# Kernel optimization log

Measured on AMD Instinct MI355X. Metric: run time of the kernel, lower is better.

The kernel has to match this reference:

```python
import jax, jax.numpy as jnp
import numpy as np

B, S = 256, 512
MEM, DK, DV, DS = 32, 128, 128, 256
NQ = 10000
ABILITY_SCALE = 3.0


def _kaiming(key, shape, fan_in):
    return jax.random.normal(key, shape, dtype=jnp.float32) * jnp.sqrt(2.0 / fan_in)


def setup_inputs() -> dict:
    key = jax.random.key(0)
    ks = jax.random.split(key, 20)
    q_data = jax.random.randint(ks[0], (B, S), 0, NQ + 1)
    qa_data = jax.random.randint(ks[1], (B, S), 0, 2 * NQ + 1)
    # embedding tables (padding_idx=0 row zeroed)
    q_table = _kaiming(ks[2], (NQ + 1, DK), DK).at[0].set(0.0)
    qa_table = _kaiming(ks[3], (2 * NQ + 1, DV), DV).at[0].set(0.0)
    # DKVMN memories
    key_memory = _kaiming(ks[4], (MEM, DK), DK)
    init_value_memory = _kaiming(ks[5], (MEM, DV), DV)
    # DKVMN write transforms (erase: sigmoid, add: tanh)
    W_erase = _kaiming(ks[6], (DV, DV), DV); b_erase = jnp.zeros((DV,), jnp.float32)
    W_add = _kaiming(ks[7], (DV, DV), DV); b_add = jnp.zeros((DV,), jnp.float32)
    # summary network: Linear(DV+DK -> DS) + tanh
    W_sum = _kaiming(ks[8], (DV + DK, DS), DV + DK); b_sum = jnp.zeros((DS,), jnp.float32)
    # student ability net: Linear(DS->DS)+tanh, Linear(DS->1)
    W_ab1 = _kaiming(ks[9], (DS, DS), DS); b_ab1 = jnp.zeros((DS,), jnp.float32)
    W_ab2 = _kaiming(ks[10], (DS, 1), DS); b_ab2 = jnp.zeros((1,), jnp.float32)
    # item difficulty net: Linear(DK->DK)+tanh, Linear(DK->1)
    W_df1 = _kaiming(ks[11], (DK, DK), DK); b_df1 = jnp.zeros((DK,), jnp.float32)
    W_df2 = _kaiming(ks[12], (DK, 1), DK); b_df2 = jnp.zeros((1,), jnp.float32)
    return dict(q_data=q_data, qa_data=qa_data, q_table=q_table, qa_table=qa_table,
                key_memory=key_memory, init_value_memory=init_value_memory,
                W_erase=W_erase, b_erase=b_erase, W_add=W_add, b_add=b_add,
                W_sum=W_sum, b_sum=b_sum, W_ab1=W_ab1, b_ab1=b_ab1,
                W_ab2=W_ab2, b_ab2=b_ab2, W_df1=W_df1, b_df1=b_df1,
                W_df2=W_df2, b_df2=b_df2)


def _forward(q_data, qa_data, q_table, qa_table, key_memory, init_value_memory,
             W_erase, b_erase, W_add, b_add, W_sum, b_sum,
             W_ab1, b_ab1, W_ab2, b_ab2, W_df1, b_df1, W_df2, b_df2):
    qe = q_table[q_data]            # [B,S,DK]
    qae = qa_table[qa_data]         # [B,S,DV]
    # attention weights for every timestep (depend only on q embeddings)
    w_all = jax.nn.softmax(jnp.einsum('bsd,md->bsm', qe, key_memory), axis=-1)  # [B,S,M]
    erase = jax.nn.sigmoid(qae @ W_erase + b_erase)   # [B,S,DV]
    add = jnp.tanh(qae @ W_add + b_add)               # [B,S,DV]
    Mv0 = jnp.broadcast_to(init_value_memory, (q_data.shape[0], MEM, DV))

    def step(Mv, xs):
        w, e, a = xs  # [B,M], [B,DV], [B,DV]
        read = jnp.einsum('bm,bmd->bd', w, Mv)  # read BEFORE write
        Mv = Mv * (1.0 - w[:, :, None] * e[:, None, :]) + w[:, :, None] * a[:, None, :]
        return Mv, read

    xs = (jnp.swapaxes(w_all, 0, 1), jnp.swapaxes(erase, 0, 1), jnp.swapaxes(add, 0, 1))
    _, reads = jax.lax.scan(step, Mv0, xs)          # reads: [S,B,DV]
    reads = jnp.swapaxes(reads, 0, 1)               # [B,S,DV]

    summary = jnp.tanh(jnp.concatenate([reads, qe], axis=-1) @ W_sum + b_sum)  # [B,S,DS]
    ability = jnp.tanh(summary @ W_ab1 + b_ab1) @ W_ab2 + b_ab2                # [B,S,1]
    difficulty = jnp.tanh(qe @ W_df1 + b_df1) @ W_df2 + b_df2                  # [B,S,1]
    z = ABILITY_SCALE * ability - difficulty
    pred = jax.nn.sigmoid(z)
    return (pred[..., 0], ability[..., 0], difficulty[..., 0], z[..., 0])


def reference(q_data, qa_data, q_table, qa_table, key_memory, init_value_memory,
              W_erase, b_erase, W_add, b_add, W_sum, b_sum,
              W_ab1, b_ab1, W_ab2, b_ab2, W_df1, b_df1, W_df2, b_df2):
    return _forward(q_data, qa_data, q_table, qa_table, key_memory, init_value_memory,
                    W_erase, b_erase, W_add, b_add, W_sum, b_sum,
                    W_ab1, b_ab1, W_ab2, b_ab2, W_df1, b_df1, W_df2, b_df2)
```

## Files before the change

### kernel.cpp

```cpp
#include <hip/hip_runtime.h>
#include <hip/hip_bf16.h>

typedef unsigned short u16;
typedef unsigned int   u32;

#define B_N   256
#define S_N   512
#define BSN   (B_N * S_N)
#define MEMN  32
#define DKN   128
#define DVN   128
#define DSN   256

typedef __attribute__((ext_vector_type(8))) short bf16x8;
typedef __attribute__((ext_vector_type(4))) float f32x4;

__device__ __forceinline__ float bf2f(u16 u) {
  union { u32 i; float f; } v; v.i = ((u32)u) << 16; return v.f;
}
__device__ __forceinline__ u16 f2bf(float f) {
  union { float f; u32 i; } v; v.f = f;
  u32 x = v.i;
  x += 0x7fffu + ((x >> 16) & 1u);
  return (u16)(x >> 16);
}
__device__ __forceinline__ u32 pack2(float a, float b) {
  return (u32)f2bf(a) | ((u32)f2bf(b) << 16);
}
__device__ __forceinline__ float sigmoid_fast(float x) { return 1.f / (1.f + __expf(-x)); }
__device__ __forceinline__ float tanh_fast(float x)    { return 1.f - 2.f / (__expf(2.f * x) + 1.f); }

#define GLOAD_LDS16(g, l)                                         \
  __builtin_amdgcn_global_load_lds(                               \
      (const __attribute__((address_space(1))) void*)(g),         \
      (__attribute__((address_space(3))) void*)(l), 16, 0, 0)

__global__ __launch_bounds__(256) void kPrep(
    const float* __restrict__ W_sum, const float* __restrict__ W_ab1,
    const float* __restrict__ W_er,  const float* __restrict__ W_ad,
    const float* __restrict__ key_mem, const float* __restrict__ W_df1,
    u16* __restrict__ WsumT, u16* __restrict__ Wab1T,
    u16* __restrict__ WerT,  u16* __restrict__ WaddT,
    u16* __restrict__ BqT)
{
  int e = blockIdx.x * 256 + threadIdx.x;
  if (e < 65536) {
    const int n = e >> 8, k = e & 255;
    WsumT[e] = f2bf(W_sum[k * 256 + n]);
  } else if (e < 131072) {
    e -= 65536;
    const int n = e >> 8, k = e & 255;
    Wab1T[e] = f2bf(W_ab1[k * 256 + n]);
  } else if (e < 147456) {
    e -= 131072;
    const int n = e >> 7, k = e & 127;
    WerT[e] = f2bf(W_er[k * 128 + n]);
  } else if (e < 163840) {
    e -= 147456;
    const int n = e >> 7, k = e & 127;
    WaddT[e] = f2bf(W_ad[k * 128 + n]);
  } else if (e < 184320) {
    e -= 163840;
    const int n = e >> 7, k = e & 127;
    BqT[e] = f2bf(n < 32 ? key_mem[n * 128 + k] : W_df1[k * 128 + (n - 32)]);
  }
}

__global__ __launch_bounds__(256) void kErAdd(
    const int* __restrict__ qa_data, const float* __restrict__ qa_table,
    const u16* __restrict__ WerT, const u16* __restrict__ WaddT,
    const float* __restrict__ b_er, const float* __restrict__ b_ad,
    u16* __restrict__ eras, u16* __restrict__ addb)
{
  __shared__ __align__(16) u16 As[4 * 128 * 32];
  __shared__ __align__(16) u16 Bs[2 * 128 * 32];
  const int tid = threadIdx.x;
  const int p0  = blockIdx.x * 128;
  const int sel = blockIdx.y;
  const u16*   Wt = sel ? WaddT : WerT;
  const float* bb = sel ? b_ad  : b_er;
  u16*       outp = sel ? addb  : eras;

  {
    const int r = tid >> 1, h = tid & 1;
    const long base = (long)qa_data[p0 + r] * DVN + h * 64;
    #pragma unroll
    for (int g = 0; g < 8; ++g) {
      const int k0 = h * 64 + g * 8;
      const float4 fa = *(const float4*)(qa_table + base + g * 8);
      const float4 fb = *(const float4*)(qa_table + base + g * 8 + 4);
      uint4 pk;
      pk.x = pack2(fa.x, fa.y); pk.y = pack2(fa.z, fa.w);
      pk.z = pack2(fb.x, fb.y); pk.w = pack2(fb.z, fb.w);
      *(uint4*)(As + (k0 >> 5) * 4096 + r * 32 + (k0 & 31)) = pk;
    }
  }
  {
    #pragma unroll
    for (int u = 0; u < 2; ++u) {
      const int f = tid + 256 * u;
      const int n = f >> 2, j = f & 3;
      *(uint4*)(Bs + n * 32 + j * 8) = *(const uint4*)(Wt + n * 128 + j * 8);
    }
  }
  __syncthreads();

  const int lane = tid & 63, wave = tid >> 6;
  const int wr = (wave >> 1) * 64, wc = (wave & 1) * 64;
  const int c15 = lane & 15, q = lane >> 4;

  f32x4 acc[4][4];
  #pragma unroll
  for (int b = 0; b < 4; ++b) {
    const float bv = bb[wc + 16 * b + c15];
    #pragma unroll
    for (int a = 0; a < 4; ++a) acc[a][b] = (f32x4){bv, bv, bv, bv};
  }

  for (int c = 0; c < 4; ++c) {
    const int cur = c & 1;
    uint4 st[2];
    const bool more = (c + 1 < 4);
    if (more) {
      #pragma unroll
      for (int u = 0; u < 2; ++u) {
        const int f = tid + 256 * u;
        const int n = f >> 2, j = f & 3;
        st[u] = *(const uint4*)(Wt + n * 128 + (c + 1) * 32 + j * 8);
      }
    }
    bf16x8 af[4], bf[4];
    #pragma unroll
    for (int a = 0; a < 4; ++a)
      af[a] = *(const bf16x8*)(As + c * 4096 + (wr + 16 * a + c15) * 32 + q * 8);
    #pragma unroll
    for (int b = 0; b < 4; ++b)
      bf[b] = *(const bf16x8*)(Bs + cur * 4096 + (wc + 16 * b + c15) * 32 + q * 8);
    #pragma unroll
    for (int a = 0; a < 4; ++a)
      #pragma unroll
      for (int b = 0; b < 4; ++b)
        acc[a][b] = __builtin_amdgcn_mfma_f32_16x16x32_bf16(af[a], bf[b], acc[a][b], 0, 0, 0);
    if (more) {
      #pragma unroll
      for (int u = 0; u < 2; ++u) {
        const int f = tid + 256 * u;
        const int n = f >> 2, j = f & 3;
        *(uint4*)(Bs + (cur ^ 1) * 4096 + n * 32 + j * 8) = st[u];
      }
    }
    __syncthreads();
  }

  const int colb = wc + c15;
  #pragma unroll
  for (int a = 0; a < 4; ++a) {
    #pragma unroll
    for (int r = 0; r < 4; ++r) {
      const int row = p0 + wr + 16 * a + 4 * q + r;
      u16* yp = outp + (long)row * DVN + colb;
      #pragma unroll
      for (int b = 0; b < 4; ++b) {
        const float v = sel ? tanh_fast(acc[a][b][r]) : sigmoid_fast(acc[a][b][r]);
        yp[16 * b] = f2bf(v);
      }
    }
  }
}

__global__ __launch_bounds__(256) void kSum(
    const u16* __restrict__ X, const u16* __restrict__ WsumT,
    const float* __restrict__ bias, u16* __restrict__ Y)
{
  __shared__ __align__(16) u16 As[8 * 128 * 32];
  __shared__ __align__(16) u16 Bs[2 * 128 * 32];
  const int tid = threadIdx.x;
  const int p0  = blockIdx.x * 128;
  const int j0  = blockIdx.y * 128;

  {
    #pragma unroll
    for (int u = 0; u < 16; ++u) {
      const int f = tid + 256 * u;
      const int r = f >> 5, j = f & 31;
      const uint4 raw = *(const uint4*)(X + (long)(p0 + r) * DSN + j * 8);
      *(uint4*)(As + (j >> 2) * 4096 + r * 32 + (j & 3) * 8) = raw;
    }
  }
  {
    #pragma unroll
    for (int u = 0; u < 2; ++u) {
      const int f = tid + 256 * u;
      const int n = f >> 2, j = f & 3;
      *(uint4*)(Bs + n * 32 + j * 8) = *(const uint4*)(WsumT + (j0 + n) * 256 + j * 8);
    }
  }
  __syncthreads();

  const int lane = tid & 63, wave = tid >> 6;
  const int wr = (wave >> 1) * 64, wc = (wave & 1) * 64;
  const int c15 = lane & 15, q = lane >> 4;

  f32x4 acc[4][4];
  #pragma unroll
  for (int b = 0; b < 4; ++b) {
    const float bv = bias[j0 + wc + 16 * b + c15];
    #pragma unroll
    for (int a = 0; a < 4; ++a) acc[a][b] = (f32x4){bv, bv, bv, bv};
  }

  for (int c = 0; c < 8; ++c) {
    const int cur = c & 1;
    uint4 st[2];
    const bool more = (c + 1 < 8);
    if (more) {
      #pragma unroll
      for (int u = 0; u < 2; ++u) {
        const int f = tid + 256 * u;
        const int n = f >> 2, j = f & 3;
        st[u] = *(const uint4*)(WsumT + (j0 + n) * 256 + (c + 1) * 32 + j * 8);
      }
    }
    bf16x8 af[4], bf[4];
    #pragma unroll
    for (int a = 0; a < 4; ++a)
      af[a] = *(const bf16x8*)(As + c * 4096 + (wr + 16 * a + c15) * 32 + q * 8);
    #pragma unroll
    for (int b = 0; b < 4; ++b)
      bf[b] = *(const bf16x8*)(Bs + cur * 4096 + (wc + 16 * b + c15) * 32 + q * 8);
    #pragma unroll
    for (int a = 0; a < 4; ++a)
      #pragma unroll
      for (int b = 0; b < 4; ++b)
        acc[a][b] = __builtin_amdgcn_mfma_f32_16x16x32_bf16(af[a], bf[b], acc[a][b], 0, 0, 0);
    if (more) {
      #pragma unroll
      for (int u = 0; u < 2; ++u) {
        const int f = tid + 256 * u;
        const int n = f >> 2, j = f & 3;
        *(uint4*)(Bs + (cur ^ 1) * 4096 + n * 32 + j * 8) = st[u];
      }
    }
    __syncthreads();
  }

  const int colb = j0 + wc + c15;
  #pragma unroll
  for (int a = 0; a < 4; ++a) {
    #pragma unroll
    for (int r = 0; r < 4; ++r) {
      const int row = p0 + wr + 16 * a + 4 * q + r;
      u16* yp = Y + (long)row * DSN + colb;
      #pragma unroll
      for (int b = 0; b < 4; ++b)
        yp[16 * b] = f2bf(tanh_fast(acc[a][b][r]));
    }
  }
}

__global__ __launch_bounds__(256) void kAb(
    const u16* __restrict__ X, const u16* __restrict__ Wab1T,
    const float* __restrict__ bias, const float* __restrict__ Wab2,
    float* __restrict__ part)
{
  __shared__ __align__(16) u16 As[8 * 128 * 32];
  __shared__ __align__(16) u16 Bs[2 * 128 * 32];
  const int tid = threadIdx.x;
  const int p0  = blockIdx.x * 128;
  const int j0  = blockIdx.y * 128;

  {
    #pragma unroll
    for (int u = 0; u < 16; ++u) {
      const int f = tid + 256 * u;
      const int r = f >> 5, j = f & 31;
      const uint4 raw = *(const uint4*)(X + (long)(p0 + r) * DSN + j * 8);
      *(uint4*)(As + (j >> 2) * 4096 + r * 32 + (j & 3) * 8) = raw;
    }
  }
  {
    #pragma unroll
    for (int u = 0; u < 2; ++u) {
      const int f = tid + 256 * u;
      const int n = f >> 2, j = f & 3;
      *(uint4*)(Bs + n * 32 + j * 8) = *(const uint4*)(Wab1T + (j0 + n) * 256 + j * 8);
    }
  }
  __syncthreads();

  const int lane = tid & 63, wave = tid >> 6;
  const int wr = (wave >> 1) * 64, wc = (wave & 1) * 64;
  const int c15 = lane & 15, q = lane >> 4;

  f32x4 acc[4][4];
  float w2v[4];
  #pragma unroll
  for (int b = 0; b < 4; ++b) {
    const int col = j0 + wc + 16 * b + c15;
    const float bv = bias[col];
    w2v[b] = Wab2[col];
    #pragma unroll
    for (int a = 0; a < 4; ++a) acc[a][b] = (f32x4){bv, bv, bv, bv};
  }

  for (int c = 0; c < 8; ++c) {
    const int cur = c & 1;
    uint4 st[2];
    const bool more = (c + 1 < 8);
    if (more) {
      #pragma unroll
      for (int u = 0; u < 2; ++u) {
        const int f = tid + 256 * u;
        const int n = f >> 2, j = f & 3;
        st[u] = *(const uint4*)(Wab1T + (j0 + n) * 256 + (c + 1) * 32 + j * 8);
      }
    }
    bf16x8 af[4], bf[4];
    #pragma unroll
    for (int a = 0; a < 4; ++a)
      af[a] = *(const bf16x8*)(As + c * 4096 + (wr + 16 * a + c15) * 32 + q * 8);
    #pragma unroll
    for (int b = 0; b < 4; ++b)
      bf[b] = *(const bf16x8*)(Bs + cur * 4096 + (wc + 16 * b + c15) * 32 + q * 8);
    #pragma unroll
    for (int a = 0; a < 4; ++a)
      #pragma unroll
      for (int b = 0; b < 4; ++b)
        acc[a][b] = __builtin_amdgcn_mfma_f32_16x16x32_bf16(af[a], bf[b], acc[a][b], 0, 0, 0);
    if (more) {
      #pragma unroll
      for (int u = 0; u < 2; ++u) {
        const int f = tid + 256 * u;
        const int n = f >> 2, j = f & 3;
        *(uint4*)(Bs + (cur ^ 1) * 4096 + n * 32 + j * 8) = st[u];
      }
    }
    __syncthreads();
  }

  float sv[4][4];
  #pragma unroll
  for (int a = 0; a < 4; ++a) {
    #pragma unroll
    for (int r = 0; r < 4; ++r) {
      float s = 0.f;
      #pragma unroll
      for (int b = 0; b < 4; ++b)
        s = fmaf(tanh_fast(acc[a][b][r]), w2v[b], s);
      s += __shfl_xor(s, 1, 64);
      s += __shfl_xor(s, 2, 64);
      s += __shfl_xor(s, 4, 64);
      s += __shfl_xor(s, 8, 64);
      sv[a][r] = s;
    }
  }
  float* red = (float*)Bs;
  if ((wave & 1) && c15 == 0) {
    #pragma unroll
    for (int a = 0; a < 4; ++a)
      #pragma unroll
      for (int r = 0; r < 4; ++r)
        red[wr + 16 * a + 4 * q + r] = sv[a][r];
  }
  __syncthreads();
  if (!(wave & 1) && c15 == 0) {
    #pragma unroll
    for (int a = 0; a < 4; ++a)
      #pragma unroll
      for (int r = 0; r < 4; ++r) {
        const int rr = wr + 16 * a + 4 * q + r;
        part[(long)blockIdx.y * BSN + p0 + rr] = sv[a][r] + red[rr];
      }
  }
}

__global__ __launch_bounds__(256) void kQe(
    const int* __restrict__ q_data, const float* __restrict__ q_table,
    const u16* __restrict__ BqT,
    const float* __restrict__ bdf1, const float* __restrict__ Wdf2,
    const float* __restrict__ bdf2,
    float* __restrict__ w_all, float* __restrict__ diff,
    u16* __restrict__ sin_buf)
{
  __shared__ __align__(16) u16 As[4 * 128 * 32];
  __shared__ __align__(16) u16 Bs[4 * 160 * 32];
  const int tid = threadIdx.x;
  const int p0  = blockIdx.x * 128;

  {
    const int r = tid >> 1, h = tid & 1;
    const long base = (long)q_data[p0 + r] * DKN + h * 64;
    #pragma unroll
    for (int g = 0; g < 8; ++g) {
      const int k0 = h * 64 + g * 8;
      const float4 fa = *(const float4*)(q_table + base + g * 8);
      const float4 fb = *(const float4*)(q_table + base + g * 8 + 4);
      uint4 pk;
      pk.x = pack2(fa.x, fa.y); pk.y = pack2(fa.z, fa.w);
      pk.z = pack2(fb.x, fb.y); pk.w = pack2(fb.z, fb.w);
      *(uint4*)(As + (k0 >> 5) * 4096 + r * 32 + (k0 & 31)) = pk;
      *(uint4*)(sin_buf + (long)(p0 + r) * DSN + DKN + k0) = pk;
    }
  }
  {
    #pragma unroll
    for (int u = 0; u < 10; ++u) {
      const int f = tid + 256 * u;
      const int n = f >> 4, jj = f & 15;
      *(uint4*)(Bs + (jj >> 2) * 5120 + n * 32 + (jj & 3) * 8) =
          *(const uint4*)(BqT + n * 128 + jj * 8);
    }
  }
  __syncthreads();

  const int lane = tid & 63, wave = tid >> 6;
  const int wr = (wave >> 1) * 64, wc = (wave & 1) * 80;
  const int c15 = lane & 15, q = lane >> 4;

  f32x4 acc[4][5];
  float w2v[5];
  #pragma unroll
  for (int b = 0; b < 5; ++b) {
    const int col = wc + 16 * b + c15;
    const float bv = (col < 32) ? 0.f : bdf1[col - 32];
    w2v[b] = (col < 32) ? 0.f : Wdf2[col - 32];
    #pragma unroll
    for (int a = 0; a < 4; ++a) acc[a][b] = (f32x4){bv, bv, bv, bv};
  }

  #pragma unroll
  for (int c = 0; c < 4; ++c) {
    bf16x8 af[4], bf[5];
    #pragma unroll
    for (int a = 0; a < 4; ++a)
      af[a] = *(const bf16x8*)(As + c * 4096 + (wr + 16 * a + c15) * 32 + q * 8);
    #pragma unroll
    for (int b = 0; b < 5; ++b)
      bf[b] = *(const bf16x8*)(Bs + c * 5120 + (wc + 16 * b + c15) * 32 + q * 8);
    #pragma unroll
    for (int a = 0; a < 4; ++a)
      #pragma unroll
      for (int b = 0; b < 5; ++b)
        acc[a][b] = __builtin_amdgcn_mfma_f32_16x16x32_bf16(af[a], bf[b], acc[a][b], 0, 0, 0);
  }

  if (wc == 0) {
    #pragma unroll
    for (int a = 0; a < 4; ++a) {
      #pragma unroll
      for (int r = 0; r < 4; ++r) {
        float s0 = acc[a][0][r], s1 = acc[a][1][r];
        float mx = fmaxf(s0, s1);
        mx = fmaxf(mx, __shfl_xor(mx, 1, 64));
        mx = fmaxf(mx, __shfl_xor(mx, 2, 64));
        mx = fmaxf(mx, __shfl_xor(mx, 4, 64));
        mx = fmaxf(mx, __shfl_xor(mx, 8, 64));
        const float e0 = __expf(s0 - mx), e1 = __expf(s1 - mx);
        float sm = e0 + e1;
        sm += __shfl_xor(sm, 1, 64);
        sm += __shfl_xor(sm, 2, 64);
        sm += __shfl_xor(sm, 4, 64);
        sm += __shfl_xor(sm, 8, 64);
        const float inv = 1.f / sm;
        const int row = p0 + wr + 16 * a + 4 * q + r;
        w_all[(long)row * MEMN + c15]      = e0 * inv;
        w_all[(long)row * MEMN + 16 + c15] = e1 * inv;
      }
    }
  }

  float sv[4][4];
  #pragma unroll
  for (int a = 0; a < 4; ++a) {
    #pragma unroll
    for (int r = 0; r < 4; ++r) {
      float s = 0.f;
      #pragma unroll
      for (int b = 0; b < 5; ++b)
        s = fmaf(tanh_fast(acc[a][b][r]), w2v[b], s);
      s += __shfl_xor(s, 1, 64);
      s += __shfl_xor(s, 2, 64);
      s += __shfl_xor(s, 4, 64);
      s += __shfl_xor(s, 8, 64);
      sv[a][r] = s;
    }
  }
  __syncthreads();
  float* red = (float*)As;
  if ((wave & 1) && c15 == 0) {
    #pragma unroll
    for (int a = 0; a < 4; ++a)
      #pragma unroll
      for (int r = 0; r < 4; ++r)
        red[wr + 16 * a + 4 * q + r] = sv[a][r];
  }
  __syncthreads();
  if (!(wave & 1) && c15 == 0) {
    const float bd = bdf2[0];
    #pragma unroll
    for (int a = 0; a < 4; ++a)
      #pragma unroll
      for (int r = 0; r < 4; ++r) {
        const int rr = wr + 16 * a + 4 * q + r;
        diff[p0 + rr] = sv[a][r] + red[rr] + bd;
      }
  }
}

#define CHUNK_BYTES 12288
#define PB_OFF      25088

#define KSTAGE(K, BUF)                                                        \
  {                                                                           \
    const char* wsrc = (const char*)(w_all + (pbase + (long)(K) * 32) * MEMN);\
    const char* esrc = (const char*)(eras + (pbase + (long)(K) * 32) * DVN)   \
                       + ch * 128;                                            \
    const char* asrc = (const char*)(addb + (pbase + (long)(K) * 32) * DVN)   \
                       + ch * 128;                                            \
    char* dst = lds + (BUF) * CHUNK_BYTES;                                    \
    _Pragma("unroll")                                                         \
    for (int r = 0; r < 3; ++r) {                                             \
      const int o = (tid + r * 256) * 16;                                     \
      const char* src;                                                        \
      if (o < 4096) {                                                         \
        src = wsrc + o;                                                       \
      } else if (o < 8192) {                                                  \
        const int f = o - 4096;                                               \
        src = esrc + (f >> 7) * 256 + (f & 127);                              \
      } else {                                                                \
        const int f = o - 8192;                                               \
        src = asrc + (f >> 7) * 256 + (f & 127);                              \
      }                                                                       \
      GLOAD_LDS16(src, dst + o);                                              \
    }                                                                         \
  }

__global__ __launch_bounds__(256) void kScan(
    const float* __restrict__ w_all, const u16* __restrict__ eras,
    const u16* __restrict__ addb, const float* __restrict__ init_mem,
    u16* __restrict__ sin_buf)
{
  __shared__ __align__(16) char lds[PB_OFF + 32768];
  const int tid = threadIdx.x;
  const int ch  = blockIdx.x & 1;
  const int lc  = tid >> 2;
  const int gc  = ch * 64 + lc;
  const int h   = tid & 3;
  const long pbase = (long)(blockIdx.x >> 1) * S_N;

  float* pb = (float*)(lds + PB_OFF);

  float Mv[8];
  #pragma unroll
  for (int m = 0; m < 8; ++m) Mv[m] = init_mem[(h * 8 + m) * DVN + gc];

  const int lc2  = tid & 63;
  const int sblk = tid >> 6;
  u16* sp2 = sin_buf + pbase * DSN + ch * 64 + lc2;

  KSTAGE(0, 0)
  for (int k = 0; k < 16; ++k) {
    __syncthreads();
    if (k + 1 < 16) KSTAGE(k + 1, (k + 1) & 1)

    const char*  wb  = lds + (k & 1) * CHUNK_BYTES;
    const f32x4* wl4 = (const f32x4*)wb;
    const u16*   el  = (const u16*)(wb + 4096);
    const u16*   al  = (const u16*)(wb + 8192);

    f32x4 Wr[3][2];
    u16 er[3], ar[3];
    #pragma unroll
    for (int i = 0; i < 2; ++i) Wr[0][i] = wl4[h * 2 + i];
    er[0] = el[lc]; ar[0] = al[lc];
    #pragma unroll
    for (int i = 0; i < 2; ++i) Wr[1][i] = wl4[8 + h * 2 + i];
    er[1] = el[64 + lc]; ar[1] = al[64 + lc];

    #pragma unroll
    for (int s = 0; s < 32; ++s) {
      const int cur = s % 3, nx2 = (s + 2) % 3;
      Wr[nx2][0] = wl4[(s + 2) * 8 + h * 2];
      Wr[nx2][1] = wl4[(s + 2) * 8 + h * 2 + 1];
      er[nx2] = el[(s + 2) * 64 + lc];
      ar[nx2] = al[(s + 2) * 64 + lc];
      {
        float ac0 = 0.f, ac1 = 0.f, ac2 = 0.f, ac3 = 0.f;
        #pragma unroll
        for (int i = 0; i < 2; ++i) {
          ac0 = fmaf(Wr[cur][i][0], Mv[4 * i + 0], ac0);
          ac1 = fmaf(Wr[cur][i][1], Mv[4 * i + 1], ac1);
          ac2 = fmaf(Wr[cur][i][2], Mv[4 * i + 2], ac2);
          ac3 = fmaf(Wr[cur][i][3], Mv[4 * i + 3], ac3);
        }
        pb[s * 256 + lc * 4 + h] = (ac0 + ac1) + (ac2 + ac3);
        const float ec = bf2f(er[cur]);
        const float an = -bf2f(ar[cur]);
        #pragma unroll
        for (int i = 0; i < 2; ++i) {
          #pragma unroll
          for (int j = 0; j < 4; ++j) {
            const float t = fmaf(ec, Mv[4 * i + j], an);
            Mv[4 * i + j] = fmaf(-Wr[cur][i][j], t, Mv[4 * i + j]);
          }
        }
      }
    }

    __syncthreads();
    const int lb = k * 32;
    #pragma unroll
    for (int r = 0; r < 8; ++r) {
      const int s = sblk * 8 + r;
      const f32x4 pv = *(const f32x4*)(pb + s * 256 + lc2 * 4);
      sp2[(long)(lb + s) * DSN] = f2bf((pv[0] + pv[1]) + (pv[2] + pv[3]));
    }
  }
}

__global__ __launch_bounds__(256) void kOut(
    const float* __restrict__ part, const float* __restrict__ diff,
    const float* __restrict__ bab2, float* __restrict__ out)
{
  const int p = blockIdx.x * 256 + threadIdx.x;
  const float ab = part[p] + part[BSN + p] + bab2[0];
  const float d  = diff[p];
  const float z  = 3.0f * ab - d;
  out[p]           = sigmoid_fast(z);
  out[BSN + p]     = ab;
  out[2 * BSN + p] = d;
  out[3 * BSN + p] = z;
}

extern "C" void kernel_launch(void* const* d_in, const int* in_sizes, int n_in,
                              void* d_out, int out_size, void* d_ws, size_t ws_size,
                              hipStream_t stream)
{
  const int*   q_data   = (const int*)d_in[0];
  const int*   qa_data  = (const int*)d_in[1];
  const float* q_table  = (const float*)d_in[2];
  const float* qa_table = (const float*)d_in[3];
  const float* key_mem  = (const float*)d_in[4];
  const float* init_mem = (const float*)d_in[5];
  const float* W_erase  = (const float*)d_in[6];
  const float* b_erase  = (const float*)d_in[7];
  const float* W_add    = (const float*)d_in[8];
  const float* b_add    = (const float*)d_in[9];
  const float* W_sum    = (const float*)d_in[10];
  const float* b_sum    = (const float*)d_in[11];
  const float* W_ab1    = (const float*)d_in[12];
  const float* b_ab1    = (const float*)d_in[13];
  const float* W_ab2    = (const float*)d_in[14];
  const float* b_ab2    = (const float*)d_in[15];
  const float* W_df1    = (const float*)d_in[16];
  const float* b_df1    = (const float*)d_in[17];
  const float* W_df2    = (const float*)d_in[18];
  const float* b_df2    = (const float*)d_in[19];

  char* ws = (char*)d_ws;
  float* w_all = (float*)(ws + 0);
  u16*   eras  = (u16*)(ws + 16777216);
  u16*   addb  = (u16*)(ws + 50331648);
  u16*   sinb  = (u16*)(ws + 83886080);
  float* diffb = (float*)(ws + 150994944);
  float* part  = (float*)(ws + 151519232);
  u16*   WerT  = (u16*)(ws + 152567808);
  u16*   WaddT = (u16*)(ws + 152600576);
  u16*   WsumT = (u16*)(ws + 152633344);
  u16*   Wab1T = (u16*)(ws + 152764416);
  u16*   BqT   = (u16*)(ws + 152895488);
  u16*   summ  = eras;

  kPrep<<<dim3(720), 256, 0, stream>>>(W_sum, W_ab1, W_erase, W_add, key_mem, W_df1,
                                       WsumT, Wab1T, WerT, WaddT, BqT);
  kErAdd<<<dim3(BSN / 128, 2), 256, 0, stream>>>(qa_data, qa_table, WerT, WaddT,
                                                 b_erase, b_add, eras, addb);
  kQe<<<dim3(BSN / 128), 256, 0, stream>>>(q_data, q_table, BqT, b_df1, W_df2, b_df2,
                                           w_all, diffb, sinb);
  kScan<<<dim3(B_N * 2), 256, 0, stream>>>(w_all, eras, addb, init_mem, sinb);
  kSum<<<dim3(BSN / 128, 2), 256, 0, stream>>>(sinb, WsumT, b_sum, summ);
  kAb<<<dim3(BSN / 128, 2), 256, 0, stream>>>(summ, Wab1T, b_ab1, W_ab2, part);
  kOut<<<dim3(BSN / 256), 256, 0, stream>>>(part, diffb, b_ab2, (float*)d_out);
}
```

Measured before the change: 353.1 us.

## Fuse summary, ability and output kernels; compute erase and add in one block

The summary GEMM, ability GEMM and output epilogue are merged into one kernel that keeps the 128x256 tanh summary tile in shared memory and reuses it as the A operand of the second GEMM. This removes the global round trip of the summary activations and the partial-sum buffer, and drops two launches. Separately, kErAdd now loops over erase and add inside each block so the gathered qa embeddings are loaded once instead of twice. The trade-offs are higher register pressure (32 accumulators per wave), single-buffered weight staging with an extra barrier per k-step, and half as many blocks.

```diff
diff --git a/kernel.cpp b/kernel.cpp
--- a/kernel.cpp
+++ b/kernel.cpp
@@ -76,10 +76,6 @@
   __shared__ __align__(16) u16 Bs[2 * 128 * 32];
   const int tid = threadIdx.x;
   const int p0  = blockIdx.x * 128;
-  const int sel = blockIdx.y;
-  const u16*   Wt = sel ? WaddT : WerT;
-  const float* bb = sel ? b_ad  : b_er;
-  u16*       outp = sel ? addb  : eras;
 
   {
     const int r = tid >> 1, h = tid & 1;
@@ -95,282 +91,83 @@
       *(uint4*)(As + (k0 >> 5) * 4096 + r * 32 + (k0 & 31)) = pk;
     }
   }
-  {
-    #pragma unroll
-    for (int u = 0; u < 2; ++u) {
-      const int f = tid + 256 * u;
-      const int n = f >> 2, j = f & 3;
-      *(uint4*)(Bs + n * 32 + j * 8) = *(const uint4*)(Wt + n * 128 + j * 8);
-    }
-  }
-  __syncthreads();
 
   const int lane = tid & 63, wave = tid >> 6;
   const int wr = (wave >> 1) * 64, wc = (wave & 1) * 64;
   const int c15 = lane & 15, q = lane >> 4;
 
-  f32x4 acc[4][4];
-  #pragma unroll
-  for (int b = 0; b < 4; ++b) {
-    const float bv = bb[wc + 16 * b + c15];
-    #pragma unroll
-    for (int a = 0; a < 4; ++a) acc[a][b] = (f32x4){bv, bv, bv, bv};
-  }
-
-  for (int c = 0; c < 4; ++c) {
-    const int cur = c & 1;
-    uint4 st[2];
-    const bool more = (c + 1 < 4);
-    if (more) {
+  for (int sel = 0; sel < 2; ++sel) {
+    const u16*   Wt = sel ? WaddT : WerT;
+    const float* bb = sel ? b_ad  : b_er;
+    u16*       outp = sel ? addb  : eras;
+
+    {
       #pragma unroll
       for (int u = 0; u < 2; ++u) {
         const int f = tid + 256 * u;
         const int n = f >> 2, j = f & 3;
-        st[u] = *(const uint4*)(Wt + n * 128 + (c + 1) * 32 + j * 8);
-      }
-    }
-    bf16x8 af[4], bf[4];
-    #pragma unroll
-    for (int a = 0; a < 4; ++a)
-      af[a] = *(const bf16x8*)(As + c * 4096 + (wr + 16 * a + c15) * 32 + q * 8);
-    #pragma unroll
-    for (int b = 0; b < 4; ++b)
-      bf[b] = *(const bf16x8*)(Bs + cur * 4096 + (wc + 16 * b + c15) * 32 + q * 8);
-    #pragma unroll
-    for (int a = 0; a < 4; ++a)
+        *(uint4*)(Bs + n * 32 + j * 8) = *(const uint4*)(Wt + n * 128 + j * 8);
+      }
+    }
+    __syncthreads();
+
+    f32x4 acc[4][4];
+    #pragma unroll
+    for (int b = 0; b < 4; ++b) {
+      const float bv = bb[wc + 16 * b + c15];
+      #pragma unroll
+      for (int a = 0; a < 4; ++a) acc[a][b] = (f32x4){bv, bv, bv, bv};
+    }
+
+    for (int c = 0; c < 4; ++c) {
+      const int cur = c & 1;
+      uint4 st[2];
+      const bool more = (c + 1 < 4);
+      if (more) {
+        #pragma unroll
+        for (int u = 0; u < 2; ++u) {
+          const int f = tid + 256 * u;
+          const int n = f >> 2, j = f & 3;
+          st[u] = *(const uint4*)(Wt + n * 128 + (c + 1) * 32 + j * 8);
+        }
+      }
+      bf16x8 af[4], bf[4];
+      #pragma unroll
+      for (int a = 0; a < 4; ++a)
+        af[a] = *(const bf16x8*)(As + c * 4096 + (wr + 16 * a + c15) * 32 + q * 8);
       #pragma unroll
       for (int b = 0; b < 4; ++b)
-        acc[a][b] = __builtin_amdgcn_mfma_f32_16x16x32_bf16(af[a], bf[b], acc[a][b], 0, 0, 0);
-    if (more) {
-      #pragma unroll
-      for (int u = 0; u < 2; ++u) {
-        const int f = tid + 256 * u;
-        const int n = f >> 2, j = f & 3;
-        *(uint4*)(Bs + (cur ^ 1) * 4096 + n * 32 + j * 8) = st[u];
-      }
-    }
-    __syncthreads();
-  }
-
-  const int colb = wc + c15;
-  #pragma unroll
-  for (int a = 0; a < 4; ++a) {
-    #pragma unroll
-    for (int r = 0; r < 4; ++r) {
-      const int row = p0 + wr + 16 * a + 4 * q + r;
-      u16* yp = outp + (long)row * DVN + colb;
-      #pragma unroll
-      for (int b = 0; b < 4; ++b) {
-        const float v = sel ? tanh_fast(acc[a][b][r]) : sigmoid_fast(acc[a][b][r]);
-        yp[16 * b] = f2bf(v);
-      }
-    }
-  }
-}
-
-__global__ __launch_bounds__(256) void kSum(
-    const u16* __restrict__ X, const u16* __restrict__ WsumT,
-    const float* __restrict__ bias, u16* __restrict__ Y)
-{
-  __shared__ __align__(16) u16 As[8 * 128 * 32];
-  __shared__ __align__(16) u16 Bs[2 * 128 * 32];
-  const int tid = threadIdx.x;
-  const int p0  = blockIdx.x * 128;
-  const int j0  = blockIdx.y * 128;
-
-  {
-    #pragma unroll
-    for (int u = 0; u < 16; ++u) {
-      const int f = tid + 256 * u;
-      const int r = f >> 5, j = f & 31;
-      const uint4 raw = *(const uint4*)(X + (long)(p0 + r) * DSN + j * 8);
-      *(uint4*)(As + (j >> 2) * 4096 + r * 32 + (j & 3) * 8) = raw;
-    }
-  }
-  {
-    #pragma unroll
-    for (int u = 0; u < 2; ++u) {
-      const int f = tid + 256 * u;
-      const int n = f >> 2, j = f & 3;
-      *(uint4*)(Bs + n * 32 + j * 8) = *(const uint4*)(WsumT + (j0 + n) * 256 + j * 8);
-    }
-  }
-  __syncthreads();
-
-  const int lane = tid & 63, wave = tid >> 6;
-  const int wr = (wave >> 1) * 64, wc = (wave & 1) * 64;
-  const int c15 = lane & 15, q = lane >> 4;
-
-  f32x4 acc[4][4];
-  #pragma unroll
-  for (int b = 0; b < 4; ++b) {
-    const float bv = bias[j0 + wc + 16 * b + c15];
-    #pragma unroll
-    for (int a = 0; a < 4; ++a) acc[a][b] = (f32x4){bv, bv, bv, bv};
-  }
-
-  for (int c = 0; c < 8; ++c) {
-    const int cur = c & 1;
-    uint4 st[2];
-    const bool more = (c + 1 < 8);
-    if (more) {
-      #pragma unroll
-      for (int u = 0; u < 2; ++u) {
-        const int f = tid + 256 * u;
-        const int n = f >> 2, j = f & 3;
-        st[u] = *(const uint4*)(WsumT + (j0 + n) * 256 + (c + 1) * 32 + j * 8);
-      }
-    }
-    bf16x8 af[4], bf[4];
-    #pragma unroll
-    for (int a = 0; a < 4; ++a)
-      af[a] = *(const bf16x8*)(As + c * 4096 + (wr + 16 * a + c15) * 32 + q * 8);
-    #pragma unroll
-    for (int b = 0; b < 4; ++b)
-      bf[b] = *(const bf16x8*)(Bs + cur * 4096 + (wc + 16 * b + c15) * 32 + q * 8);
-    #pragma unroll
-    for (int a = 0; a < 4; ++a)
-      #pragma unroll
-      for (int b = 0; b < 4; ++b)
-        acc[a][b] = __builtin_amdgcn_mfma_f32_16x16x32_bf16(af[a], bf[b], acc[a][b], 0, 0, 0);
-    if (more) {
-      #pragma unroll
-      for (int u = 0; u < 2; ++u) {
-        const int f = tid + 256 * u;
-        const int n = f >> 2, j = f & 3;
-        *(uint4*)(Bs + (cur ^ 1) * 4096 + n * 32 + j * 8) = st[u];
-      }
-    }
-    __syncthreads();
-  }
-
-  const int colb = j0 + wc + c15;
-  #pragma unroll
-  for (int a = 0; a < 4; ++a) {
-    #pragma unroll
-    for (int r = 0; r < 4; ++r) {
-      const int row = p0 + wr + 16 * a + 4 * q + r;
-      u16* yp = Y + (long)row * DSN + colb;
-      #pragma unroll
-      for (int b = 0; b < 4; ++b)
-        yp[16 * b] = f2bf(tanh_fast(acc[a][b][r]));
-    }
-  }
-}
-
-__global__ __launch_bounds__(256) void kAb(
-    const u16* __restrict__ X, const u16* __restrict__ Wab1T,
-    const float* __restrict__ bias, const float* __restrict__ Wab2,
-    float* __restrict__ part)
-{
-  __shared__ __align__(16) u16 As[8 * 128 * 32];
-  __shared__ __align__(16) u16 Bs[2 * 128 * 32];
-  const int tid = threadIdx.x;
-  const int p0  = blockIdx.x * 128;
-  const int j0  = blockIdx.y * 128;
-
-  {
-    #pragma unroll
-    for (int u = 0; u < 16; ++u) {
-      const int f = tid + 256 * u;
-      const int r = f >> 5, j = f & 31;
-      const uint4 raw = *(const uint4*)(X + (long)(p0 + r) * DSN + j * 8);
-      *(uint4*)(As + (j >> 2) * 4096 + r * 32 + (j & 3) * 8) = raw;
-    }
-  }
-  {
-    #pragma unroll
-    for (int u = 0; u < 2; ++u) {
-      const int f = tid + 256 * u;
-      const int n = f >> 2, j = f & 3;
-      *(uint4*)(Bs + n * 32 + j * 8) = *(const uint4*)(Wab1T + (j0 + n) * 256 + j * 8);
-    }
-  }
-  __syncthreads();
-
-  const int lane = tid & 63, wave = tid >> 6;
-  const int wr = (wave >> 1) * 64, wc = (wave & 1) * 64;
-  const int c15 = lane & 15, q = lane >> 4;
-
-  f32x4 acc[4][4];
-  float w2v[4];
-  #pragma unroll
-  for (int b = 0; b < 4; ++b) {
-    const int col = j0 + wc + 16 * b + c15;
-    const float bv = bias[col];
-    w2v[b] = Wab2[col];
-    #pragma unroll
-    for (int a = 0; a < 4; ++a) acc[a][b] = (f32x4){bv, bv, bv, bv};
-  }
-
-  for (int c = 0; c < 8; ++c) {
-    const int cur = c & 1;
-    uint4 st[2];
-    const bool more = (c + 1 < 8);
-    if (more) {
-      #pragma unroll
-      for (int u = 0; u < 2; ++u) {
-        const int f = tid + 256 * u;
-        const int n = f >> 2, j = f & 3;
-        st[u] = *(const uint4*)(Wab1T + (j0 + n) * 256 + (c + 1) * 32 + j * 8);
-      }
-    }
-    bf16x8 af[4], bf[4];
-    #pragma unroll
-    for (int a = 0; a < 4; ++a)
-      af[a] = *(const bf16x8*)(As + c * 4096 + (wr + 16 * a + c15) * 32 + q * 8);
-    #pragma unroll
-    for (int b = 0; b < 4; ++b)
-      bf[b] = *(const bf16x8*)(Bs + cur * 4096 + (wc + 16 * b + c15) * 32 + q * 8);
-    #pragma unroll
-    for (int a = 0; a < 4; ++a)
-      #pragma unroll
-      for (int b = 0; b < 4; ++b)
-        acc[a][b] = __builtin_amdgcn_mfma_f32_16x16x32_bf16(af[a], bf[b], acc[a][b], 0, 0, 0);
-    if (more) {
-      #pragma unroll
-      for (int u = 0; u < 2; ++u) {
-        const int f = tid + 256 * u;
-        const int n = f >> 2, j = f & 3;
-        *(uint4*)(Bs + (cur ^ 1) * 4096 + n * 32 + j * 8) = st[u];
-      }
-    }
-    __syncthreads();
-  }
-
-  float sv[4][4];
-  #pragma unroll
-  for (int a = 0; a < 4; ++a) {
-    #pragma unroll
-    for (int r = 0; r < 4; ++r) {
-      float s = 0.f;
-      #pragma unroll
-      for (int b = 0; b < 4; ++b)
-        s = fmaf(tanh_fast(acc[a][b][r]), w2v[b], s);
-      s += __shfl_xor(s, 1, 64);
-      s += __shfl_xor(s, 2, 64);
-      s += __shfl_xor(s, 4, 64);
-      s += __shfl_xor(s, 8, 64);
-      sv[a][r] = s;
-    }
-  }
-  float* red = (float*)Bs;
-  if ((wave & 1) && c15 == 0) {
-    #pragma unroll
-    for (int a = 0; a < 4; ++a)
-      #pragma unroll
-      for (int r = 0; r < 4; ++r)
-        red[wr + 16 * a + 4 * q + r] = sv[a][r];
-  }
-  __syncthreads();
-  if (!(wave & 1) && c15 == 0) {
-    #pragma unroll
-    for (int a = 0; a < 4; ++a)
+        bf[b] = *(const bf16x8*)(Bs + cur * 4096 + (wc + 16 * b + c15) * 32 + q * 8);
+      #pragma unroll
+      for (int a = 0; a < 4; ++a)
+        #pragma unroll
+        for (int b = 0; b < 4; ++b)
+          acc[a][b] = __builtin_amdgcn_mfma_f32_16x16x32_bf16(af[a], bf[b], acc[a][b], 0, 0, 0);
+      if (more) {
+        #pragma unroll
+        for (int u = 0; u < 2; ++u) {
+          const int f = tid + 256 * u;
+          const int n = f >> 2, j = f & 3;
+          *(uint4*)(Bs + (cur ^ 1) * 4096 + n * 32 + j * 8) = st[u];
+        }
+      }
+      __syncthreads();
+    }
+
+    const int colb = wc + c15;
+    #pragma unroll
+    for (int a = 0; a < 4; ++a) {
       #pragma unroll
       for (int r = 0; r < 4; ++r) {
-        const int rr = wr + 16 * a + 4 * q + r;
-        part[(long)blockIdx.y * BSN + p0 + rr] = sv[a][r] + red[rr];
-      }
+        const int row = p0 + wr + 16 * a + 4 * q + r;
+        u16* yp = outp + (long)row * DVN + colb;
+        #pragma unroll
+        for (int b = 0; b < 4; ++b) {
+          const float v = sel ? tanh_fast(acc[a][b][r]) : sigmoid_fast(acc[a][b][r]);
+          yp[16 * b] = f2bf(v);
+        }
+      }
+    }
   }
 }
 
@@ -618,18 +415,192 @@
   }
 }
 
-__global__ __launch_bounds__(256) void kOut(
-    const float* __restrict__ part, const float* __restrict__ diff,
-    const float* __restrict__ bab2, float* __restrict__ out)
+__global__ __launch_bounds__(256) void kSumAb(
+    const u16* __restrict__ X, const u16* __restrict__ WsumT,
+    const float* __restrict__ bsum, const u16* __restrict__ Wab1T,
+    const float* __restrict__ bab1, const float* __restrict__ Wab2,
+    const float* __restrict__ bab2, const float* __restrict__ diffb,
+    float* __restrict__ out)
 {
-  const int p = blockIdx.x * 256 + threadIdx.x;
-  const float ab = part[p] + part[BSN + p] + bab2[0];
-  const float d  = diff[p];
-  const float z  = 3.0f * ab - d;
-  out[p]           = sigmoid_fast(z);
-  out[BSN + p]     = ab;
-  out[2 * BSN + p] = d;
-  out[3 * BSN + p] = z;
+  __shared__ __align__(16) u16 As[8 * 128 * 32];
+  __shared__ __align__(16) u16 Bs[256 * 32];
+  const int tid = threadIdx.x;
+  const int p0  = blockIdx.x * 128;
+
+  {
+    #pragma unroll
+    for (int u = 0; u < 16; ++u) {
+      const int f = tid + 256 * u;
+      const int r = f >> 5, j = f & 31;
+      const uint4 raw = *(const uint4*)(X + (long)(p0 + r) * DSN + j * 8);
+      *(uint4*)(As + (j >> 2) * 4096 + r * 32 + (j & 3) * 8) = raw;
+    }
+  }
+  {
+    #pragma unroll
+    for (int u = 0; u < 4; ++u) {
+      const int f = tid + 256 * u;
+      const int n = f >> 2, j = f & 3;
+      *(uint4*)(Bs + n * 32 + j * 8) = *(const uint4*)(WsumT + n * 256 + j * 8);
+    }
+  }
+  __syncthreads();
+
+  const int lane = tid & 63, wave = tid >> 6;
+  const int wr = (wave >> 1) * 64, wc = (wave & 1) * 128;
+  const int c15 = lane & 15, q = lane >> 4;
+
+  f32x4 acc[4][8];
+  #pragma unroll
+  for (int b = 0; b < 8; ++b) {
+    const float bv = bsum[wc + 16 * b + c15];
+    #pragma unroll
+    for (int a = 0; a < 4; ++a) acc[a][b] = (f32x4){bv, bv, bv, bv};
+  }
+
+  for (int c = 0; c < 8; ++c) {
+    uint4 st[4];
+    const bool more = (c + 1 < 8);
+    if (more) {
+      #pragma unroll
+      for (int u = 0; u < 4; ++u) {
+        const int f = tid + 256 * u;
+        const int n = f >> 2, j = f & 3;
+        st[u] = *(const uint4*)(WsumT + n * 256 + (c + 1) * 32 + j * 8);
+      }
+    }
+    bf16x8 af[4], bf[8];
+    #pragma unroll
+    for (int a = 0; a < 4; ++a)
+      af[a] = *(const bf16x8*)(As + c * 4096 + (wr + 16 * a + c15) * 32 + q * 8);
+    #pragma unroll
+    for (int b = 0; b < 8; ++b)
+      bf[b] = *(const bf16x8*)(Bs + (wc + 16 * b + c15) * 32 + q * 8);
+    #pragma unroll
+    for (int a = 0; a < 4; ++a)
+      #pragma unroll
+      for (int b = 0; b < 8; ++b)
+        acc[a][b] = __builtin_amdgcn_mfma_f32_16x16x32_bf16(af[a], bf[b], acc[a][b], 0, 0, 0);
+    __syncthreads();
+    if (more) {
+      #pragma unroll
+      for (int u = 0; u < 4; ++u) {
+        const int f = tid + 256 * u;
+        const int n = f >> 2, j = f & 3;
+        *(uint4*)(Bs + n * 32 + j * 8) = st[u];
+      }
+      __syncthreads();
+    }
+  }
+
+  #pragma unroll
+  for (int a = 0; a < 4; ++a)
+    #pragma unroll
+    for (int b = 0; b < 8; ++b) {
+      const int col = wc + 16 * b + c15;
+      u16* sp = As + (col >> 5) * 4096 + (col & 31);
+      #pragma unroll
+      for (int r = 0; r < 4; ++r) {
+        const int row = wr + 16 * a + 4 * q + r;
+        sp[row * 32] = f2bf(tanh_fast(acc[a][b][r]));
+      }
+    }
+  {
+    #pragma unroll
+    for (int u = 0; u < 4; ++u) {
+      const int f = tid + 256 * u;
+      const int n = f >> 2, j = f & 3;
+      *(uint4*)(Bs + n * 32 + j * 8) = *(const uint4*)(Wab1T + n * 256 + j * 8);
+    }
+  }
+  __syncthreads();
+
+  float w2v[8];
+  #pragma unroll
+  for (int b = 0; b < 8; ++b) {
+    const int col = wc + 16 * b + c15;
+    const float bv = bab1[col];
+    w2v[b] = Wab2[col];
+    #pragma unroll
+    for (int a = 0; a < 4; ++a) acc[a][b] = (f32x4){bv, bv, bv, bv};
+  }
+  for (int c = 0; c < 8; ++c) {
+    uint4 st[4];
+    const bool more = (c + 1 < 8);
+    if (more) {
+      #pragma unroll
+      for (int u = 0; u < 4; ++u) {
+        const int f = tid + 256 * u;
+        const int n = f >> 2, j = f & 3;
+        st[u] = *(const uint4*)(Wab1T + n * 256 + (c + 1) * 32 + j * 8);
+      }
+    }
+    bf16x8 af[4], bf[8];
+    #pragma unroll
+    for (int a = 0; a < 4; ++a)
+      af[a] = *(const bf16x8*)(As + c * 4096 + (wr + 16 * a + c15) * 32 + q * 8);
+    #pragma unroll
+    for (int b = 0; b < 8; ++b)
+      bf[b] = *(const bf16x8*)(Bs + (wc + 16 * b + c15) * 32 + q * 8);
+    #pragma unroll
+    for (int a = 0; a < 4; ++a)
+      #pragma unroll
+      for (int b = 0; b < 8; ++b)
+        acc[a][b] = __builtin_amdgcn_mfma_f32_16x16x32_bf16(af[a], bf[b], acc[a][b], 0, 0, 0);
+    __syncthreads();
+    if (more) {
+      #pragma unroll
+      for (int u = 0; u < 4; ++u) {
+        const int f = tid + 256 * u;
+        const int n = f >> 2, j = f & 3;
+        *(uint4*)(Bs + n * 32 + j * 8) = st[u];
+      }
+      __syncthreads();
+    }
+  }
+
+  float sv[4][4];
+  #pragma unroll
+  for (int a = 0; a < 4; ++a) {
+    #pragma unroll
+    for (int r = 0; r < 4; ++r) {
+      float s = 0.f;
+      #pragma unroll
+      for (int b = 0; b < 8; ++b)
+        s = fmaf(tanh_fast(acc[a][b][r]), w2v[b], s);
+      s += __shfl_xor(s, 1, 64);
+      s += __shfl_xor(s, 2, 64);
+      s += __shfl_xor(s, 4, 64);
+      s += __shfl_xor(s, 8, 64);
+      sv[a][r] = s;
+    }
+  }
+  float* red = (float*)Bs;
+  if ((wave & 1) && c15 == 0) {
+    #pragma unroll
+    for (int a = 0; a < 4; ++a)
+      #pragma unroll
+      for (int r = 0; r < 4; ++r)
+        red[wr + 16 * a + 4 * q + r] = sv[a][r];
+  }
+  __syncthreads();
+  if (!(wave & 1) && c15 == 0) {
+    const float bb = bab2[0];
+    #pragma unroll
+    for (int a = 0; a < 4; ++a)
+      #pragma unroll
+      for (int r = 0; r < 4; ++r) {
+        const int rr = wr + 16 * a + 4 * q + r;
+        const int p  = p0 + rr;
+        const float ab = sv[a][r] + red[rr] + bb;
+        const float d  = diffb[p];
+        const float z  = 3.0f * ab - d;
+        out[p]           = sigmoid_fast(z);
+        out[BSN + p]     = ab;
+        out[2 * BSN + p] = d;
+        out[3 * BSN + p] = z;
+      }
+  }
 }
 
 extern "C" void kernel_launch(void* const* d_in, const int* in_sizes, int n_in,
@@ -663,22 +634,19 @@
   u16*   addb  = (u16*)(ws + 50331648);
   u16*   sinb  = (u16*)(ws + 83886080);
   float* diffb = (float*)(ws + 150994944);
-  float* part  = (float*)(ws + 151519232);
   u16*   WerT  = (u16*)(ws + 152567808);
   u16*   WaddT = (u16*)(ws + 152600576);
   u16*   WsumT = (u16*)(ws + 152633344);
   u16*   Wab1T = (u16*)(ws + 152764416);
   u16*   BqT   = (u16*)(ws + 152895488);
-  u16*   summ  = eras;
 
   kPrep<<<dim3(720), 256, 0, stream>>>(W_sum, W_ab1, W_erase, W_add, key_mem, W_df1,
                                        WsumT, Wab1T, WerT, WaddT, BqT);
-  kErAdd<<<dim3(BSN / 128, 2), 256, 0, stream>>>(qa_data, qa_table, WerT, WaddT,
-                                                 b_erase, b_add, eras, addb);
+  kErAdd<<<dim3(BSN / 128), 256, 0, stream>>>(qa_data, qa_table, WerT, WaddT,
+                                              b_erase, b_add, eras, addb);
   kQe<<<dim3(BSN / 128), 256, 0, stream>>>(q_data, q_table, BqT, b_df1, W_df2, b_df2,
                                            w_all, diffb, sinb);
   kScan<<<dim3(B_N * 2), 256, 0, stream>>>(w_all, eras, addb, init_mem, sinb);
-  kSum<<<dim3(BSN / 128, 2), 256, 0, stream>>>(sinb, WsumT, b_sum, summ);
-  kAb<<<dim3(BSN / 128, 2), 256, 0, stream>>>(summ, Wab1T, b_ab1, W_ab2, part);
-  kOut<<<dim3(BSN / 256), 256, 0, stream>>>(part, diffb, b_ab2, (float*)d_out);
-}
+  kSumAb<<<dim3(BSN / 128), 256, 0, stream>>>(sinb, WsumT, b_sum, Wab1T, b_ab1,
+                                              W_ab2, b_ab2, diffb, (float*)d_out);
+}
```

Result: slower. 569.0 us (+61.2%).
